# Performance work log

Hardware: AMD Instinct MI355X
Metric: run time of the kernel (lower is better)

Reference implementation:

```python
import jax, jax.numpy as jnp
import numpy as np

N = 50000          # nodes
E = 1600000        # edges (avg degree 32)
IN_NODE = 256
IN_EDGE = 64
H = 128            # node_h_dim
EH = 32            # edge_h_dim
L = 3              # layer_num


def _layernorm(x, g, b, eps=1e-5):
    m = jnp.mean(x, axis=-1, keepdims=True)
    v = jnp.var(x, axis=-1, keepdims=True)
    return (x - m) * jax.lax.rsqrt(v + eps) * g + b


def setup_inputs() -> dict:
    key = jax.random.key(0)
    ks = jax.random.split(key, 16)
    def g(k, shape, scale=0.02):
        return jax.random.normal(k, shape, dtype=jnp.float32) * scale
    return {
        "node_features": g(ks[0], (N, IN_NODE), 1.0),
        "edge_index": jax.random.randint(ks[1], (2, E), 0, N, dtype=jnp.int32),
        "edge_attr": g(ks[2], (E, IN_EDGE), 1.0),
        # input projections
        "Wn": g(ks[3], (IN_NODE, H)), "bn": jnp.zeros((H,), jnp.float32),
        "We": g(ks[4], (IN_EDGE, EH)), "be": jnp.zeros((EH,), jnp.float32),
        # per-layer ResGatedGraphConv params (stacked over L layers)
        "Wk": g(ks[5], (L, H, H)), "bk": jnp.zeros((L, H), jnp.float32),
        "Wq": g(ks[6], (L, H, H)), "bq": jnp.zeros((L, H), jnp.float32),
        "Wv": g(ks[7], (L, H, H)), "bv": jnp.zeros((L, H), jnp.float32),
        "Wed": g(ks[8], (L, EH, H)), "bed": jnp.zeros((L, H), jnp.float32),
        "Wskip": g(ks[9], (L, H, H)),              # lin_skip, bias=False
        "cb": jnp.zeros((L, H), jnp.float32),       # conv final bias
        "ln_g": jnp.ones((L, H), jnp.float32), "ln_b": jnp.zeros((L, H), jnp.float32),
        # concat-hidden projection
        "Wh": g(ks[10], (L * H, H)), "bh": jnp.zeros((H,), jnp.float32),
    }


def reference(node_features, edge_index, edge_attr, Wn, bn, We, be,
              Wk, bk, Wq, bq, Wv, bv, Wed, bed, Wskip, cb, ln_g, ln_b, Wh, bh):
    src, dst = edge_index[0], edge_index[1]  # messages flow src -> dst
    x = node_features @ Wn + bn              # [N, H]
    e = edge_attr @ We + be                  # [E, EH]
    hidden_states = []
    for i in range(L):  # fixed layer count
        k = x @ Wk[i] + bk[i]                # key on target nodes
        q = x @ Wq[i] + bq[i]                # query on source nodes
        v = x @ Wv[i] + bv[i]
        el = e @ Wed[i] + bed[i]             # [E, H]
        gate = jax.nn.sigmoid(k[dst] + q[src] + el)
        msg = gate * v[src]                  # [E, H]
        agg = jax.ops.segment_sum(msg, dst, num_segments=N)
        h = agg + x @ Wskip[i] + cb[i]
        # dropout p=0.1 is identity in eval mode
        h = _layernorm(h, ln_g[i], ln_b[i])
        hidden_states.append(h)
        x = h
    idg_hidden = jnp.concatenate(hidden_states, axis=-1)  # [N, L*H]
    return idg_hidden @ Wh + bh
```

## Files before the change

kernel.cpp:

```cpp
#include <hip/hip_runtime.h>
#include <hip/hip_bf16.h>
#include <math.h>

#define N_NODES 50000
#define N_EDGES 1600000

struct GemmBatch {
  const float* W[4];
  const float* b[4];
  float* out[4];
};

template<int K>
__global__ __launch_bounds__(256) void gemm128(const float* __restrict__ A, int lda, int M,
                                               GemmBatch gb) {
  const float* __restrict__ W    = gb.W[blockIdx.z];
  const float* __restrict__ bias = gb.b[blockIdx.z];
  float* __restrict__ out        = gb.out[blockIdx.z];
  __shared__ float xT[32][68];
  int tid = threadIdx.x;
  int tc = tid & 31, tr = tid >> 5;
  int rbase = blockIdx.x * 64;
  float acc[8][4];
  #pragma unroll
  for (int i = 0; i < 8; i++)
    #pragma unroll
    for (int m = 0; m < 4; m++) acc[i][m] = 0.f;

  for (int kc = 0; kc < K; kc += 32) {
    {
      int c = tid & 31, rg = tid >> 5;
      #pragma unroll
      for (int i = 0; i < 8; i++) {
        int r = rg * 8 + i;
        int row = rbase + r; if (row >= M) row = M - 1;
        xT[c][r] = A[(size_t)row * lda + kc + c];
      }
    }
    __syncthreads();
    #pragma unroll
    for (int k = 0; k < 32; k++) {
      float4 x0 = *(const float4*)&xT[k][tr * 8];
      float4 x1 = *(const float4*)&xT[k][tr * 8 + 4];
      float w[4];
      #pragma unroll
      for (int m = 0; m < 4; m++) w[m] = W[(size_t)(kc + k) * 128 + tc + 32 * m];
      float xr[8] = {x0.x, x0.y, x0.z, x0.w, x1.x, x1.y, x1.z, x1.w};
      #pragma unroll
      for (int i = 0; i < 8; i++)
        #pragma unroll
        for (int m = 0; m < 4; m++)
          acc[i][m] = fmaf(xr[i], w[m], acc[i][m]);
    }
    __syncthreads();
  }
  #pragma unroll
  for (int m = 0; m < 4; m++) {
    float bb = bias[tc + 32 * m];
    #pragma unroll
    for (int i = 0; i < 8; i++) {
      int row = rbase + tr * 8 + i;
      if (row < M) out[(size_t)row * 128 + tc + 32 * m] = acc[i][m] + bb;
    }
  }
}

template<int K>
__global__ __launch_bounds__(256) void gemm32(const float* __restrict__ A, int lda, int M,
                                              const float* __restrict__ W,
                                              const float* __restrict__ bias,
                                              float* __restrict__ out) {
  __shared__ float xT[32][132];
  int tid = threadIdx.x;
  int tc = tid & 31, tr = tid >> 5;
  int rbase = blockIdx.x * 128;
  float acc[16];
  #pragma unroll
  for (int i = 0; i < 16; i++) acc[i] = 0.f;

  for (int kc = 0; kc < K; kc += 32) {
    {
      int c = tid & 31, rg = tid >> 5;
      #pragma unroll
      for (int i = 0; i < 16; i++) {
        int r = rg * 16 + i;
        int row = rbase + r; if (row >= M) row = M - 1;
        xT[c][r] = A[(size_t)row * lda + kc + c];
      }
    }
    __syncthreads();
    #pragma unroll
    for (int k = 0; k < 32; k++) {
      float w = W[(size_t)(kc + k) * 32 + tc];
      #pragma unroll
      for (int u = 0; u < 4; u++) {
        float4 xv = *(const float4*)&xT[k][tr * 16 + 4 * u];
        acc[4*u+0] = fmaf(xv.x, w, acc[4*u+0]);
        acc[4*u+1] = fmaf(xv.y, w, acc[4*u+1]);
        acc[4*u+2] = fmaf(xv.z, w, acc[4*u+2]);
        acc[4*u+3] = fmaf(xv.w, w, acc[4*u+3]);
      }
    }
    __syncthreads();
  }
  float bb = bias[tc];
  #pragma unroll
  for (int i = 0; i < 16; i++) {
    int row = rbase + tr * 16 + i;
    if (row < M) out[(size_t)row * 32 + tc] = acc[i] + bb;
  }
}

__global__ __launch_bounds__(256) void edge_kernel(const float* __restrict__ e,
    const int* __restrict__ src, const int* __restrict__ dst,
    const float* __restrict__ kf, const float* __restrict__ qf, const float* __restrict__ vf,
    const float* __restrict__ Wed, const float* __restrict__ bed,
    float* __restrict__ agg, int nE) {
  __shared__ float wlds[32 * 128];
  int tid = threadIdx.x;
  #pragma unroll
  for (int t = 0; t < 16; t++) wlds[tid + 256 * t] = Wed[tid + 256 * t];
  __syncthreads();
  int j = tid & 127;
  int sub = tid >> 7;
  float bj = bed[j];
  for (int eid = blockIdx.x * 2 + sub; eid < nE; eid += gridDim.x * 2) {
    int s = src[eid], d = dst[eid];
    const float4* er = (const float4*)(e + (size_t)eid * 32);
    float el = bj;
    #pragma unroll
    for (int t = 0; t < 8; t++) {
      float4 ev = er[t];
      el = fmaf(ev.x, wlds[(4*t+0)*128 + j], el);
      el = fmaf(ev.y, wlds[(4*t+1)*128 + j], el);
      el = fmaf(ev.z, wlds[(4*t+2)*128 + j], el);
      el = fmaf(ev.w, wlds[(4*t+3)*128 + j], el);
    }
    float kd = kf[(size_t)d * 128 + j];
    float qs = qf[(size_t)s * 128 + j];
    float vs = vf[(size_t)s * 128 + j];
    float t  = kd + qs + el;
    float u  = __expf(-t);
    float g  = __builtin_amdgcn_rcpf(1.0f + u);
    atomicAdd(&agg[(size_t)d * 128 + j], g * vs);
  }
}

__global__ __launch_bounds__(256) void ln_kernel(const float* __restrict__ agg,
    const float* __restrict__ g, const float* __restrict__ b,
    float* __restrict__ out, int ldo, int M) {
  int tid = threadIdx.x;
  int lane = tid & 63;
  int row = blockIdx.x * 4 + (tid >> 6);
  if (row >= M) return;
  float a0 = agg[(size_t)row * 128 + lane];
  float a1 = agg[(size_t)row * 128 + 64 + lane];
  float s = a0 + a1, ss = a0 * a0 + a1 * a1;
  #pragma unroll
  for (int off = 32; off; off >>= 1) {
    s  += __shfl_xor(s, off);
    ss += __shfl_xor(ss, off);
  }
  float mean = s * (1.f / 128.f);
  float var  = ss * (1.f / 128.f) - mean * mean;
  float rstd = rsqrtf(var + 1e-5f);
  float h0 = (a0 - mean) * rstd * g[lane] + b[lane];
  float h1 = (a1 - mean) * rstd * g[lane + 64] + b[lane + 64];
  out[(size_t)row * ldo + lane]      = h0;
  out[(size_t)row * ldo + lane + 64] = h1;
}

extern "C" void kernel_launch(void* const* d_in, const int* in_sizes, int n_in,
                              void* d_out, int out_size, void* d_ws, size_t ws_size,
                              hipStream_t stream) {
  const float* nf  = (const float*)d_in[0];
  const int*   ei  = (const int*)  d_in[1];
  const float* ea  = (const float*)d_in[2];
  const float* Wn  = (const float*)d_in[3];
  const float* bn  = (const float*)d_in[4];
  const float* We  = (const float*)d_in[5];
  const float* be  = (const float*)d_in[6];
  const float* Wk  = (const float*)d_in[7];
  const float* bk  = (const float*)d_in[8];
  const float* Wq  = (const float*)d_in[9];
  const float* bq  = (const float*)d_in[10];
  const float* Wv  = (const float*)d_in[11];
  const float* bv  = (const float*)d_in[12];
  const float* Wed = (const float*)d_in[13];
  const float* bed = (const float*)d_in[14];
  const float* Wsk = (const float*)d_in[15];
  const float* cb  = (const float*)d_in[16];
  const float* lng = (const float*)d_in[17];
  const float* lnb = (const float*)d_in[18];
  const float* Wh  = (const float*)d_in[19];
  const float* bh  = (const float*)d_in[20];
  float* out = (float*)d_out;

  float* ws  = (float*)d_ws;
  float* x0  = ws;
  float* e   = x0  + (size_t)N_NODES * 128;
  float* kf  = e   + (size_t)N_EDGES * 32;
  float* qf  = kf  + (size_t)N_NODES * 128;
  float* vf  = qf  + (size_t)N_NODES * 128;
  float* agg = vf  + (size_t)N_NODES * 128;
  float* hid = agg + (size_t)N_NODES * 128;

  const int* srcp = ei;
  const int* dstp = ei + N_EDGES;

  dim3 blk(256);
  int gN = (N_NODES + 63) / 64;

  { GemmBatch gb{}; gb.W[0] = Wn; gb.b[0] = bn; gb.out[0] = x0;
    gemm128<256><<<dim3(gN, 1, 1), blk, 0, stream>>>(nf, 256, N_NODES, gb); }

  gemm32<64><<<dim3(N_EDGES / 128), blk, 0, stream>>>(ea, 64, N_EDGES, We, be, e);

  const float* xcur = x0; int ldx = 128;
  for (int i = 0; i < 3; i++) {
    GemmBatch gb{};
    gb.W[0] = Wk  + (size_t)i * 128 * 128; gb.b[0] = bk + i * 128; gb.out[0] = kf;
    gb.W[1] = Wq  + (size_t)i * 128 * 128; gb.b[1] = bq + i * 128; gb.out[1] = qf;
    gb.W[2] = Wv  + (size_t)i * 128 * 128; gb.b[2] = bv + i * 128; gb.out[2] = vf;
    gb.W[3] = Wsk + (size_t)i * 128 * 128; gb.b[3] = cb + i * 128; gb.out[3] = agg;
    gemm128<128><<<dim3(gN, 1, 4), blk, 0, stream>>>(xcur, ldx, N_NODES, gb);

    edge_kernel<<<dim3(2048), blk, 0, stream>>>(e, srcp, dstp, kf, qf, vf,
        Wed + (size_t)i * 32 * 128, bed + i * 128, agg, N_EDGES);

    ln_kernel<<<dim3((N_NODES + 3) / 4), blk, 0, stream>>>(agg, lng + i * 128,
        lnb + i * 128, hid + i * 128, 384, N_NODES);

    xcur = hid + i * 128; ldx = 384;
  }

  { GemmBatch gb{}; gb.W[0] = Wh; gb.b[0] = bh; gb.out[0] = out;
    gemm128<384><<<dim3(gN, 1, 1), blk, 0, stream>>>(hid, 384, N_NODES, gb); }
}
```

Measured before the change: 4.382 ms.

## Sort edges into CSR by destination and fuse aggregation with layernorm

```diff
diff --git a/kernel.cpp b/kernel.cpp
--- a/kernel.cpp
+++ b/kernel.cpp
@@ -66,10 +66,11 @@
 }
 
 template<int K>
-__global__ __launch_bounds__(256) void gemm32(const float* __restrict__ A, int lda, int M,
-                                              const float* __restrict__ W,
-                                              const float* __restrict__ bias,
-                                              float* __restrict__ out) {
+__global__ __launch_bounds__(256) void gemm32_scatter(const float* __restrict__ A, int lda, int M,
+                                                      const float* __restrict__ W,
+                                                      const float* __restrict__ bias,
+                                                      const int* __restrict__ epos,
+                                                      float* __restrict__ out) {
   __shared__ float xT[32][132];
   int tid = threadIdx.x;
   int tc = tid & 31, tr = tid >> 5;
@@ -107,67 +108,136 @@
   #pragma unroll
   for (int i = 0; i < 16; i++) {
     int row = rbase + tr * 16 + i;
-    if (row < M) out[(size_t)row * 32 + tc] = acc[i] + bb;
-  }
-}
-
-__global__ __launch_bounds__(256) void edge_kernel(const float* __restrict__ e,
-    const int* __restrict__ src, const int* __restrict__ dst,
-    const float* __restrict__ kf, const float* __restrict__ qf, const float* __restrict__ vf,
+    if (row < M) {
+      int orow = epos[row];
+      out[(size_t)orow * 32 + tc] = acc[i] + bb;
+    }
+  }
+}
+
+__global__ __launch_bounds__(256) void zero_deg(int* __restrict__ deg, int n) {
+  int i = blockIdx.x * 256 + threadIdx.x;
+  if (i < n) deg[i] = 0;
+}
+
+__global__ __launch_bounds__(256) void hist_kernel(const int* __restrict__ dst,
+                                                   int* __restrict__ deg, int nE) {
+  int i = blockIdx.x * 256 + threadIdx.x;
+  if (i < nE) atomicAdd(&deg[dst[i]], 1);
+}
+
+__global__ __launch_bounds__(1024) void scan_kernel(const int* __restrict__ deg,
+                                                    int* __restrict__ rowptr,
+                                                    int* __restrict__ cursor, int n) {
+  __shared__ int part[1024];
+  int tid = threadIdx.x;
+  const int CH = (n + 1023) / 1024;
+  int base = tid * CH;
+  int sum = 0;
+  for (int i = 0; i < CH; i++) if (base + i < n) sum += deg[base + i];
+  part[tid] = sum;
+  __syncthreads();
+  for (int off = 1; off < 1024; off <<= 1) {
+    int v = (tid >= off) ? part[tid - off] : 0;
+    __syncthreads();
+    part[tid] += v;
+    __syncthreads();
+  }
+  int run = (tid == 0) ? 0 : part[tid - 1];
+  for (int i = 0; i < CH; i++) {
+    int idx = base + i;
+    if (idx < n) { rowptr[idx] = run; cursor[idx] = run; run += deg[idx]; }
+  }
+  if (tid == 1023) rowptr[n] = part[1023];
+}
+
+__global__ __launch_bounds__(256) void scatter_kernel(const int* __restrict__ src,
+                                                      const int* __restrict__ dst,
+                                                      int* __restrict__ cursor,
+                                                      int* __restrict__ srcs,
+                                                      int* __restrict__ epos, int nE) {
+  int eid = blockIdx.x * 256 + threadIdx.x;
+  if (eid < nE) {
+    int d = dst[eid];
+    int pos = atomicAdd(&cursor[d], 1);
+    srcs[pos] = src[eid];
+    epos[eid] = pos;
+  }
+}
+
+__global__ __launch_bounds__(256) void agg_ln_kernel(
+    const float* __restrict__ e_s, const int* __restrict__ srcs,
+    const int* __restrict__ rowptr,
+    const float* __restrict__ kf, const float* __restrict__ qf,
+    const float* __restrict__ vf, const float* __restrict__ skip,
     const float* __restrict__ Wed, const float* __restrict__ bed,
-    float* __restrict__ agg, int nE) {
+    const float* __restrict__ g, const float* __restrict__ b,
+    float* __restrict__ out, int ldo, int M) {
   __shared__ float wlds[32 * 128];
+  __shared__ float red[2][2][2];
   int tid = threadIdx.x;
   #pragma unroll
   for (int t = 0; t < 16; t++) wlds[tid + 256 * t] = Wed[tid + 256 * t];
   __syncthreads();
-  int j = tid & 127;
+
+  int j   = tid & 127;
   int sub = tid >> 7;
+  int node = blockIdx.x * 2 + sub;
   float bj = bed[j];
-  for (int eid = blockIdx.x * 2 + sub; eid < nE; eid += gridDim.x * 2) {
-    int s = src[eid], d = dst[eid];
-    const float4* er = (const float4*)(e + (size_t)eid * 32);
-    float el = bj;
-    #pragma unroll
-    for (int t = 0; t < 8; t++) {
-      float4 ev = er[t];
-      el = fmaf(ev.x, wlds[(4*t+0)*128 + j], el);
-      el = fmaf(ev.y, wlds[(4*t+1)*128 + j], el);
-      el = fmaf(ev.z, wlds[(4*t+2)*128 + j], el);
-      el = fmaf(ev.w, wlds[(4*t+3)*128 + j], el);
-    }
-    float kd = kf[(size_t)d * 128 + j];
-    float qs = qf[(size_t)s * 128 + j];
-    float vs = vf[(size_t)s * 128 + j];
-    float t  = kd + qs + el;
-    float u  = __expf(-t);
-    float g  = __builtin_amdgcn_rcpf(1.0f + u);
-    atomicAdd(&agg[(size_t)d * 128 + j], g * vs);
-  }
-}
-
-__global__ __launch_bounds__(256) void ln_kernel(const float* __restrict__ agg,
-    const float* __restrict__ g, const float* __restrict__ b,
-    float* __restrict__ out, int ldo, int M) {
-  int tid = threadIdx.x;
-  int lane = tid & 63;
-  int row = blockIdx.x * 4 + (tid >> 6);
-  if (row >= M) return;
-  float a0 = agg[(size_t)row * 128 + lane];
-  float a1 = agg[(size_t)row * 128 + 64 + lane];
-  float s = a0 + a1, ss = a0 * a0 + a1 * a1;
+  float acc = 0.f;
+  float hval = 0.f;
+
+  if (node < M) {
+    int p0 = rowptr[node], p1 = rowptr[node + 1];
+    float kd = kf[(size_t)node * 128 + j];
+    float qs = 0.f, vs = 0.f;
+    if (p0 < p1) {
+      int s0 = srcs[p0];
+      qs = qf[(size_t)s0 * 128 + j];
+      vs = vf[(size_t)s0 * 128 + j];
+    }
+    for (int p = p0; p < p1; p++) {
+      float qn = 0.f, vn = 0.f;
+      if (p + 1 < p1) {
+        int sn = srcs[p + 1];
+        qn = qf[(size_t)sn * 128 + j];
+        vn = vf[(size_t)sn * 128 + j];
+      }
+      const float4* er = (const float4*)(e_s + (size_t)p * 32);
+      float el = bj;
+      #pragma unroll
+      for (int t = 0; t < 8; t++) {
+        float4 ev = er[t];
+        el = fmaf(ev.x, wlds[(4*t+0)*128 + j], el);
+        el = fmaf(ev.y, wlds[(4*t+1)*128 + j], el);
+        el = fmaf(ev.z, wlds[(4*t+2)*128 + j], el);
+        el = fmaf(ev.w, wlds[(4*t+3)*128 + j], el);
+      }
+      float t_  = kd + qs + el;
+      float u   = __expf(-t_);
+      float gsg = __builtin_amdgcn_rcpf(1.0f + u);
+      acc = fmaf(gsg, vs, acc);
+      qs = qn; vs = vn;
+    }
+    hval = acc + skip[(size_t)node * 128 + j];
+  }
+
+  float s = hval, ss = hval * hval;
   #pragma unroll
   for (int off = 32; off; off >>= 1) {
     s  += __shfl_xor(s, off);
     ss += __shfl_xor(ss, off);
   }
-  float mean = s * (1.f / 128.f);
-  float var  = ss * (1.f / 128.f) - mean * mean;
+  int wv = (tid >> 6) & 1;
+  if ((tid & 63) == 0) { red[sub][wv][0] = s; red[sub][wv][1] = ss; }
+  __syncthreads();
+  float S  = red[sub][0][0] + red[sub][1][0];
+  float SS = red[sub][0][1] + red[sub][1][1];
+  float mean = S * (1.f / 128.f);
+  float var  = SS * (1.f / 128.f) - mean * mean;
   float rstd = rsqrtf(var + 1e-5f);
-  float h0 = (a0 - mean) * rstd * g[lane] + b[lane];
-  float h1 = (a1 - mean) * rstd * g[lane + 64] + b[lane + 64];
-  out[(size_t)row * ldo + lane]      = h0;
-  out[(size_t)row * ldo + lane + 64] = h1;
+  if (node < M)
+    out[(size_t)node * ldo + j] = (hval - mean) * rstd * g[j] + b[j];
 }
 
 extern "C" void kernel_launch(void* const* d_in, const int* in_sizes, int n_in,
@@ -198,23 +268,34 @@
 
   float* ws  = (float*)d_ws;
   float* x0  = ws;
-  float* e   = x0  + (size_t)N_NODES * 128;
-  float* kf  = e   + (size_t)N_EDGES * 32;
+  float* e_s = x0  + (size_t)N_NODES * 128;
+  float* kf  = e_s + (size_t)N_EDGES * 32;
   float* qf  = kf  + (size_t)N_NODES * 128;
   float* vf  = qf  + (size_t)N_NODES * 128;
   float* agg = vf  + (size_t)N_NODES * 128;
   float* hid = agg + (size_t)N_NODES * 128;
+  int*   ip  = (int*)(hid + (size_t)N_NODES * 384);
+  int* deg    = ip;
+  int* rowptr = deg + N_NODES;
+  int* cursor = rowptr + N_NODES + 1;
+  int* srcs   = cursor + N_NODES;
+  int* epos   = srcs + N_EDGES;
 
   const int* srcp = ei;
   const int* dstp = ei + N_EDGES;
 
   dim3 blk(256);
   int gN = (N_NODES + 63) / 64;
+  int gE = (N_EDGES + 255) / 256;
+
+  zero_deg<<<dim3((N_NODES + 255) / 256), blk, 0, stream>>>(deg, N_NODES);
+  hist_kernel<<<dim3(gE), blk, 0, stream>>>(dstp, deg, N_EDGES);
+  scan_kernel<<<dim3(1), dim3(1024), 0, stream>>>(deg, rowptr, cursor, N_NODES);
+  scatter_kernel<<<dim3(gE), blk, 0, stream>>>(srcp, dstp, cursor, srcs, epos, N_EDGES);
 
   { GemmBatch gb{}; gb.W[0] = Wn; gb.b[0] = bn; gb.out[0] = x0;
     gemm128<256><<<dim3(gN, 1, 1), blk, 0, stream>>>(nf, 256, N_NODES, gb); }
-
-  gemm32<64><<<dim3(N_EDGES / 128), blk, 0, stream>>>(ea, 64, N_EDGES, We, be, e);
+  gemm32_scatter<64><<<dim3(N_EDGES / 128), blk, 0, stream>>>(ea, 64, N_EDGES, We, be, epos, e_s);
 
   const float* xcur = x0; int ldx = 128;
   for (int i = 0; i < 3; i++) {
@@ -225,11 +306,11 @@
     gb.W[3] = Wsk + (size_t)i * 128 * 128; gb.b[3] = cb + i * 128; gb.out[3] = agg;
     gemm128<128><<<dim3(gN, 1, 4), blk, 0, stream>>>(xcur, ldx, N_NODES, gb);
 
-    edge_kernel<<<dim3(2048), blk, 0, stream>>>(e, srcp, dstp, kf, qf, vf,
-        Wed + (size_t)i * 32 * 128, bed + i * 128, agg, N_EDGES);
-
-    ln_kernel<<<dim3((N_NODES + 3) / 4), blk, 0, stream>>>(agg, lng + i * 128,
-        lnb + i * 128, hid + i * 128, 384, N_NODES);
+    agg_ln_kernel<<<dim3((N_NODES + 1) / 2), blk, 0, stream>>>(
+        e_s, srcs, rowptr, kf, qf, vf, agg,
+        Wed + (size_t)i * 32 * 128, bed + i * 128,
+        lng + i * 128, lnb + i * 128,
+        hid + i * 128, 384, N_NODES);
 
     xcur = hid + i * 128; ldx = 384;
   }
```

Result: no change. 4.444 ms (+1.4%).
